# Kernel tuning notes

Measured on AMD Instinct MI355X. Metric: run time of the kernel, lower is better.

The kernel has to match this reference:

```python
import jax, jax.numpy as jnp
import numpy as np

SIZE = 1024
NUM_NODES = 32
BATCH = 2048
SCALE = float(np.sqrt(SIZE))
LN_EPS = 1e-5


def setup_inputs() -> dict:
    key = jax.random.key(0)
    k1, k2 = jax.random.split(key)
    x = jax.random.normal(k1, (BATCH, NUM_NODES), dtype=jnp.float32)
    # xavier_uniform_ for Linear(1, SIZE): bound = sqrt(6/(1+SIZE))
    bound = float(np.sqrt(6.0 / (1 + SIZE)))
    W = jax.random.uniform(k2, (SIZE, 1), dtype=jnp.float32, minval=-bound, maxval=bound)
    b = jnp.zeros((SIZE,), dtype=jnp.float32)
    gamma = jnp.ones((SIZE,), dtype=jnp.float32)
    beta = jnp.zeros((SIZE,), dtype=jnp.float32)
    return {"x": x, "W": W, "b": b, "gamma": gamma, "beta": beta}


def reference(x, W, b, gamma, beta):
    # expand_values: per-node Linear(1,size) is just a broadcast outer product
    # out[b,n,d] = x[b,n] * W[d,0] + b[d], then * sqrt(size)
    h = (x[:, :, None] * W[:, 0] + b) * SCALE  # (B, N, SIZE)
    # LayerNorm over last dim (biased variance, eps=1e-5), elementwise affine
    mean = jnp.mean(h, axis=-1, keepdims=True)
    var = jnp.mean(jnp.square(h - mean), axis=-1, keepdims=True)
    out = (h - mean) * jax.lax.rsqrt(var + LN_EPS) * gamma + beta
    # dropout is identity at inference
    return out
```

## Files before the change

kernel.cpp:

```cpp
#include <hip/hip_runtime.h>


#define D_SIZE   1024
#define N_ROWS   65536
#define SCALE_F  32.0f
#define LN_EPS_F 1e-5f

__global__ void stats_kernel(const float* __restrict__ W,
                             const float* __restrict__ bias,
                             float* __restrict__ stats) {
    int lane = threadIdx.x;
    float sW = 0.f, sW2 = 0.f, sB = 0.f, sB2 = 0.f, sWB = 0.f;
    for (int i = lane; i < D_SIZE; i += 64) {
        float w = W[i];
        float b = bias[i];
        sW  += w;
        sW2 += w * w;
        sB  += b;
        sB2 += b * b;
        sWB += w * b;
    }
    #pragma unroll
    for (int off = 32; off > 0; off >>= 1) {
        sW  += __shfl_down(sW,  off);
        sW2 += __shfl_down(sW2, off);
        sB  += __shfl_down(sB,  off);
        sB2 += __shfl_down(sB2, off);
        sWB += __shfl_down(sWB, off);
    }
    if (lane == 0) {
        const float inv_d = 1.0f / (float)D_SIZE;
        float mW = sW * inv_d;
        float mB = sB * inv_d;
        stats[0] = mW;
        stats[1] = mB;
        stats[2] = sW2 * inv_d - mW * mW;
        stats[3] = sB2 * inv_d - mB * mB;
        stats[4] = sWB * inv_d - mW * mB;
    }
}

__global__ __launch_bounds__(256, 8)
void fused_expand_ln_kernel(const float* __restrict__ x,
                            const float* __restrict__ W,
                            const float* __restrict__ bias,
                            const float* __restrict__ gamma,
                            const float* __restrict__ beta,
                            const float* __restrict__ stats,
                            float* __restrict__ out) {
    const float mW    = stats[0];
    const float mB    = stats[1];
    const float varW  = stats[2];
    const float varB  = stats[3];
    const float covWB = stats[4];

    const int d0 = threadIdx.x * 4;
    const float4 W4  = *reinterpret_cast<const float4*>(W     + d0);
    const float4 B4  = *reinterpret_cast<const float4*>(bias  + d0);
    const float4 G4  = *reinterpret_cast<const float4*>(gamma + d0);
    const float4 E4  = *reinterpret_cast<const float4*>(beta  + d0);

    for (int row = blockIdx.x; row < N_ROWS; row += gridDim.x) {
        const float xv   = x[row];
        const float mean = SCALE_F * (xv * mW + mB);
        const float var  = (SCALE_F * SCALE_F) *
                           (xv * xv * varW + 2.0f * xv * covWB + varB);
        const float inv  = rsqrtf(var + LN_EPS_F);

        float4 o;
        o.x = ((xv * W4.x + B4.x) * SCALE_F - mean) * inv * G4.x + E4.x;
        o.y = ((xv * W4.y + B4.y) * SCALE_F - mean) * inv * G4.y + E4.y;
        o.z = ((xv * W4.z + B4.z) * SCALE_F - mean) * inv * G4.z + E4.z;
        o.w = ((xv * W4.w + B4.w) * SCALE_F - mean) * inv * G4.w + E4.w;

        *reinterpret_cast<float4*>(out + (size_t)row * D_SIZE + d0) = o;
    }
}

extern "C" void kernel_launch(void* const* d_in, const int* in_sizes, int n_in,
                              void* d_out, int out_size, void* d_ws, size_t ws_size,
                              hipStream_t stream) {
    const float* x     = (const float*)d_in[0];
    const float* W     = (const float*)d_in[1];
    const float* bias  = (const float*)d_in[2];
    const float* gamma = (const float*)d_in[3];
    const float* beta  = (const float*)d_in[4];
    float* out   = (float*)d_out;
    float* stats = (float*)d_ws;

    stats_kernel<<<1, 64, 0, stream>>>(W, bias, stats);

    fused_expand_ln_kernel<<<2048, 256, 0, stream>>>(x, W, bias, gamma, beta,
                                                     stats, out);
}
```

Measured before the change: 276.8 us.

## Fuse stats reduction into main kernel, precompute affine coefficients, use nontemporal stores

Removes the separate single-wave stats kernel: every block now reduces the W/bias statistics itself with wave shuffles and a small shared-memory step. It also folds the mean subtraction and gamma into per-thread coefficients, so each output element costs two FMAs. Output is written with nontemporal stores to avoid polluting the cache. This drops one launch and the serial dependency between kernels, at the cost of redundant per-block reductions.

```diff
diff --git a/kernel.cpp b/kernel.cpp
--- a/kernel.cpp
+++ b/kernel.cpp
@@ -5,40 +5,9 @@
 #define N_ROWS   65536
 #define SCALE_F  32.0f
 #define LN_EPS_F 1e-5f
+#define GRID_N   2048
 
-__global__ void stats_kernel(const float* __restrict__ W,
-                             const float* __restrict__ bias,
-                             float* __restrict__ stats) {
-    int lane = threadIdx.x;
-    float sW = 0.f, sW2 = 0.f, sB = 0.f, sB2 = 0.f, sWB = 0.f;
-    for (int i = lane; i < D_SIZE; i += 64) {
-        float w = W[i];
-        float b = bias[i];
-        sW  += w;
-        sW2 += w * w;
-        sB  += b;
-        sB2 += b * b;
-        sWB += w * b;
-    }
-    #pragma unroll
-    for (int off = 32; off > 0; off >>= 1) {
-        sW  += __shfl_down(sW,  off);
-        sW2 += __shfl_down(sW2, off);
-        sB  += __shfl_down(sB,  off);
-        sB2 += __shfl_down(sB2, off);
-        sWB += __shfl_down(sWB, off);
-    }
-    if (lane == 0) {
-        const float inv_d = 1.0f / (float)D_SIZE;
-        float mW = sW * inv_d;
-        float mB = sB * inv_d;
-        stats[0] = mW;
-        stats[1] = mB;
-        stats[2] = sW2 * inv_d - mW * mW;
-        stats[3] = sB2 * inv_d - mB * mB;
-        stats[4] = sWB * inv_d - mW * mB;
-    }
-}
+typedef float vfloat4 __attribute__((ext_vector_type(4)));
 
 __global__ __launch_bounds__(256, 8)
 void fused_expand_ln_kernel(const float* __restrict__ x,
@@ -46,34 +15,71 @@
                             const float* __restrict__ bias,
                             const float* __restrict__ gamma,
                             const float* __restrict__ beta,
-                            const float* __restrict__ stats,
                             float* __restrict__ out) {
-    const float mW    = stats[0];
-    const float mB    = stats[1];
-    const float varW  = stats[2];
-    const float varB  = stats[3];
-    const float covWB = stats[4];
+    const int t  = threadIdx.x;
+    const int d0 = t * 4;
 
-    const int d0 = threadIdx.x * 4;
-    const float4 W4  = *reinterpret_cast<const float4*>(W     + d0);
-    const float4 B4  = *reinterpret_cast<const float4*>(bias  + d0);
-    const float4 G4  = *reinterpret_cast<const float4*>(gamma + d0);
-    const float4 E4  = *reinterpret_cast<const float4*>(beta  + d0);
+    const vfloat4 W4 = *reinterpret_cast<const vfloat4*>(W     + d0);
+    const vfloat4 B4 = *reinterpret_cast<const vfloat4*>(bias  + d0);
+    const vfloat4 G4 = *reinterpret_cast<const vfloat4*>(gamma + d0);
+    const vfloat4 E4 = *reinterpret_cast<const vfloat4*>(beta  + d0);
 
-    for (int row = blockIdx.x; row < N_ROWS; row += gridDim.x) {
-        const float xv   = x[row];
-        const float mean = SCALE_F * (xv * mW + mB);
-        const float var  = (SCALE_F * SCALE_F) *
-                           (xv * xv * varW + 2.0f * xv * covWB + varB);
-        const float inv  = rsqrtf(var + LN_EPS_F);
+    float sW  = W4.x + W4.y + W4.z + W4.w;
+    float sB  = B4.x + B4.y + B4.z + B4.w;
+    float sW2 = W4.x*W4.x + W4.y*W4.y + W4.z*W4.z + W4.w*W4.w;
+    float sB2 = B4.x*B4.x + B4.y*B4.y + B4.z*B4.z + B4.w*B4.w;
+    float sWB = W4.x*B4.x + W4.y*B4.y + W4.z*B4.z + W4.w*B4.w;
 
-        float4 o;
-        o.x = ((xv * W4.x + B4.x) * SCALE_F - mean) * inv * G4.x + E4.x;
-        o.y = ((xv * W4.y + B4.y) * SCALE_F - mean) * inv * G4.y + E4.y;
-        o.z = ((xv * W4.z + B4.z) * SCALE_F - mean) * inv * G4.z + E4.z;
-        o.w = ((xv * W4.w + B4.w) * SCALE_F - mean) * inv * G4.w + E4.w;
+    #pragma unroll
+    for (int off = 32; off > 0; off >>= 1) {
+        sW  += __shfl_down(sW,  off);
+        sB  += __shfl_down(sB,  off);
+        sW2 += __shfl_down(sW2, off);
+        sB2 += __shfl_down(sB2, off);
+        sWB += __shfl_down(sWB, off);
+    }
 
-        *reinterpret_cast<float4*>(out + (size_t)row * D_SIZE + d0) = o;
+    __shared__ float red[4][5];
+    const int wave = t >> 6;
+    if ((t & 63) == 0) {
+        red[wave][0] = sW;  red[wave][1] = sB;  red[wave][2] = sW2;
+        red[wave][3] = sB2; red[wave][4] = sWB;
+    }
+    __syncthreads();
+    sW  = red[0][0] + red[1][0] + red[2][0] + red[3][0];
+    sB  = red[0][1] + red[1][1] + red[2][1] + red[3][1];
+    sW2 = red[0][2] + red[1][2] + red[2][2] + red[3][2];
+    sB2 = red[0][3] + red[1][3] + red[2][3] + red[3][3];
+    sWB = red[0][4] + red[1][4] + red[2][4] + red[3][4];
+
+    const float inv_d  = 1.0f / (float)D_SIZE;
+    const float mW     = sW * inv_d;
+    const float mB     = sB * inv_d;
+    const float varW   = sW2 * inv_d - mW * mW;
+    const float varB   = sB2 * inv_d - mB * mB;
+    const float covWB  = sWB * inv_d - mW * mB;
+
+    vfloat4 A4, C4;
+    A4.x = (W4.x - mW) * G4.x;  C4.x = (B4.x - mB) * G4.x;
+    A4.y = (W4.y - mW) * G4.y;  C4.y = (B4.y - mB) * G4.y;
+    A4.z = (W4.z - mW) * G4.z;  C4.z = (B4.z - mB) * G4.z;
+    A4.w = (W4.w - mW) * G4.w;  C4.w = (B4.w - mB) * G4.w;
+
+    const float vscale = SCALE_F * SCALE_F;
+
+    for (int row = blockIdx.x; row < N_ROWS; row += GRID_N) {
+        const float xv  = x[row];
+        const float var = vscale * (xv * xv * varW + 2.0f * xv * covWB + varB);
+        const float s   = SCALE_F * rsqrtf(var + LN_EPS_F);
+
+        vfloat4 o;
+        o.x = fmaf(s, fmaf(xv, A4.x, C4.x), E4.x);
+        o.y = fmaf(s, fmaf(xv, A4.y, C4.y), E4.y);
+        o.z = fmaf(s, fmaf(xv, A4.z, C4.z), E4.z);
+        o.w = fmaf(s, fmaf(xv, A4.w, C4.w), E4.w);
+
+        __builtin_nontemporal_store(o, reinterpret_cast<vfloat4*>(
+            out + (size_t)row * D_SIZE + d0));
     }
 }
 
@@ -85,11 +91,8 @@
     const float* bias  = (const float*)d_in[2];
     const float* gamma = (const float*)d_in[3];
     const float* beta  = (const float*)d_in[4];
-    float* out   = (float*)d_out;
-    float* stats = (float*)d_ws;
+    float* out = (float*)d_out;
 
-    stats_kernel<<<1, 64, 0, stream>>>(W, bias, stats);
-
-    fused_expand_ln_kernel<<<2048, 256, 0, stream>>>(x, W, bias, gamma, beta,
-                                                     stats, out);
+    fused_expand_ln_kernel<<<GRID_N, 256, 0, stream>>>(x, W, bias, gamma,
+                                                       beta, out);
 }
```

After: 277.9 us. No clear change (+0.4%).
